# Kernel optimization log

Hardware: AMD Instinct MI355X
Metric: run time of the kernel (lower is better)

The kernel has to match this reference:

```python
import jax, jax.numpy as jnp
from jax import lax
import numpy as np

D = 256      # d_model
E = 512      # d_inner = expand * d_model
N = 16       # m_state
K = 4        # m_conv
R = 16       # dt_rank = ceil(D/16)
H = 8        # n_heads
DK = D // H  # d_keys
B, L = 4, 1024


def setup_inputs() -> dict:
    key = jax.random.key(0)
    ks = jax.random.split(key, 32)
    rn = lambda k, shape, s=0.02: jax.random.normal(k, shape, jnp.float32) * s
    p = {}
    for i, pre in enumerate(['f_', 'b_']):
        o = i * 8
        p[pre + 'Win'] = rn(ks[o], (D, 2 * E))
        p[pre + 'convw'] = rn(ks[o + 1], (E, K), 0.1)
        p[pre + 'convb'] = jnp.zeros((E,), jnp.float32)
        p[pre + 'Wx'] = rn(ks[o + 2], (E, R + 2 * N))
        p[pre + 'Wdt'] = rn(ks[o + 3], (R, E), 0.1)
        p[pre + 'dtb'] = jnp.full((E,), -4.6, jnp.float32)  # softplus(-4.6) ~ 0.01
        p[pre + 'Alog'] = jnp.log(jnp.tile(jnp.arange(1, N + 1, dtype=jnp.float32), (E, 1)))  # (E,N), S4D-real init
        p[pre + 'Dp'] = jnp.ones((E,), jnp.float32)
        p[pre + 'Wout'] = rn(ks[o + 4], (E, D))
    p['Wq'] = rn(ks[20], (D, D))
    p['Wk'] = rn(ks[21], (D, D))
    p['Wv'] = rn(ks[22], (D, D))
    p['Wo'] = rn(ks[23], (D, D))
    p['g_data'] = jax.random.normal(ks[24], (B, L, D), jnp.float32)
    return p


def mamba(x, Win, convw, convb, Wx, Wdt, dtb, Alog, Dp, Wout):
    """Standard Mamba block (in_proj -> causal depthwise conv -> SiLU -> selective scan -> gate -> out_proj)."""
    b = x.shape[0]
    xz = x @ Win                              # (B,L,2E)
    xc, z = xz[..., :E], xz[..., E:]
    # causal depthwise conv over time
    xt = jnp.pad(jnp.swapaxes(xc, 1, 2), ((0, 0), (0, 0), (K - 1, 0)))  # (B,E,L+K-1)
    xt = lax.conv_general_dilated(xt, convw[:, None, :], (1,), 'VALID',
                                  dimension_numbers=('NCH', 'OIH', 'NCH'),
                                  feature_group_count=E)
    xc = jax.nn.silu(jnp.swapaxes(xt + convb[None, :, None], 1, 2))     # (B,L,E)
    # input-dependent SSM params
    xdb = xc @ Wx                             # (B,L,R+2N)
    dt = jax.nn.softplus(xdb[..., :R] @ Wdt + dtb)      # (B,L,E)
    Bm = xdb[..., R:R + N]                    # (B,L,N)
    Cm = xdb[..., R + N:]                     # (B,L,N)
    A = -jnp.exp(Alog)                        # (E,N)
    dA = jnp.exp(dt[..., None] * A)                          # (B,L,E,N)
    dBx = (dt * xc)[..., None] * Bm[:, :, None, :]           # (B,L,E,N)

    def step(h, inp):
        dA_t, dBx_t, C_t = inp
        h = dA_t * h + dBx_t                 # (B,E,N)
        return h, jnp.einsum('ben,bn->be', h, C_t)

    inps = (jnp.swapaxes(dA, 0, 1), jnp.swapaxes(dBx, 0, 1), jnp.swapaxes(Cm, 0, 1))
    h0 = jnp.zeros((b, E, N), x.dtype)
    _, ys = lax.scan(step, h0, inps)          # (L,B,E)
    y = jnp.swapaxes(ys, 0, 1) + xc * Dp
    y = y * jax.nn.silu(z)
    return y @ Wout                           # (B,L,D)


def mha(x, Wq, Wk, Wv, Wo):
    b, l, _ = x.shape
    q = (x @ Wq).reshape(b, l, H, DK)
    k = (x @ Wk).reshape(b, l, H, DK)
    v = (x @ Wv).reshape(b, l, H, DK)
    scores = jnp.einsum('blhd,bshd->bhls', q, k) / jnp.sqrt(jnp.float32(DK))
    attn = jax.nn.softmax(scores, axis=-1)    # mask_flag=False -> no causal mask
    out = jnp.einsum('bhls,bshd->blhd', attn, v).reshape(b, l, D)
    return out @ Wo


def reference(g_data,
              f_Win, f_convw, f_convb, f_Wx, f_Wdt, f_dtb, f_Alog, f_Dp, f_Wout,
              b_Win, b_convw, b_convb, b_Wx, b_Wdt, b_dtb, b_Alog, b_Dp, b_Wout,
              Wq, Wk, Wv, Wo):
    fwd = mamba(g_data, f_Win, f_convw, f_convb, f_Wx, f_Wdt, f_dtb, f_Alog, f_Dp, f_Wout)
    # NOTE: source flips dims=[-1] (feature axis) -- reproduced faithfully
    bwd = jnp.flip(mamba(jnp.flip(g_data, -1), b_Win, b_convw, b_convb, b_Wx, b_Wdt, b_dtb, b_Alog, b_Dp, b_Wout), -1)
    trend = fwd + bwd + g_data
    attn = mha(trend, Wq, Wk, Wv, Wo)
    return jax.nn.gelu(attn)                  # dropout is identity in eval
```

## Files before the change

kernel.cpp:

```cpp
#include <hip/hip_runtime.h>
#include <math.h>

namespace {
typedef unsigned short ushort_t;
constexpr int cL = 1024;

using bf8   = __attribute__((ext_vector_type(8))) short;
using f32x4 = __attribute__((ext_vector_type(4))) float;
using u32x4 = __attribute__((ext_vector_type(4))) unsigned int;
using u32x2 = __attribute__((ext_vector_type(2))) unsigned int;
using fv4   = __attribute__((ext_vector_type(4))) float;

__device__ __forceinline__ float siluf(float x) { return x / (1.f + __expf(-x)); }
__device__ __forceinline__ float softplusf(float x) {
    return fmaxf(x, 0.f) + log1pf(__expf(-fabsf(x)));
}
__device__ __forceinline__ float geluf(float x) {
    float t = tanhf(0.7978845608028654f * (x + 0.044715f * x * x * x));
    return 0.5f * x * (1.f + t);
}
__device__ __forceinline__ ushort_t f2bf(float x) {
    unsigned int u = __float_as_uint(x);
    u = (u + 0x7FFFu + ((u >> 16) & 1u)) >> 16;
    return (ushort_t)u;
}
__device__ __forceinline__ float bf2f(ushort_t h) {
    return __uint_as_float(((unsigned int)h) << 16);
}
__device__ __forceinline__ void nts4(uint4 v, ushort_t* p) {
    u32x4 nv = {v.x, v.y, v.z, v.w};
    __builtin_nontemporal_store(nv, (u32x4*)p);
}
__device__ __forceinline__ void ntsf4(float4 v, float* p) {
    fv4 nv = {v.x, v.y, v.z, v.w};
    __builtin_nontemporal_store(nv, (fv4*)p);
}
__device__ __forceinline__ void nts2(unsigned int a, unsigned int b, ushort_t* p) {
    u32x2 nv = {a, b};
    __builtin_nontemporal_store(nv, (u32x2*)p);
}

enum { EPI_F32 = 0, EPI_GELU = 1, EPI_XZ = 2, EPI_PKS = 3 };

template <int EPI, int BM, int BN, int KS, bool DENSE, bool SW, bool CONVA>
__global__ __launch_bounds__(256)
void mg(const ushort_t* __restrict__ Ah, const ushort_t* __restrict__ Al, size_t sAz,
        const ushort_t* __restrict__ Bh, const ushort_t* __restrict__ Bl, size_t sBz,
        int lda, int ldb, int K,
        float* __restrict__ C, size_t sCz, int ldc, int colmax,
        ushort_t* __restrict__ o0, ushort_t* __restrict__ o1,
        ushort_t* __restrict__ o2, ushort_t* __restrict__ o3, size_t soz,
        const float* __restrict__ cw0, const float* __restrict__ cw1,
        const float* __restrict__ cb0, const float* __restrict__ cb1)
{
    constexpr int MT  = BM / 32;
    constexpr int NTT = BN / 32;
    constexpr int AGR = BM / 64;
    constexpr int BGR = BN / 64;
    __shared__ __align__(16) ushort_t smem[(BM + BN) * 64];
    ushort_t* sAh = smem;
    ushort_t* sAl = smem + BM * 32;
    ushort_t* sBh = smem + BM * 64;
    ushort_t* sBl = smem + BM * 64 + BN * 32;
    const int tid = threadIdx.x;
    const int w = tid >> 6, L = tid & 63, lm = L & 15, lq = L >> 4;
    const int row0 = (SW ? blockIdx.x : blockIdx.y) * BM;
    const int col0 = (SW ? blockIdx.y : blockIdx.x) * BN;
    const int z = blockIdx.z;
    const int dir = (KS == 2) ? (z >> 1) : z;
    const int ks  = (KS == 2) ? (z & 1) : 0;
    const int wm = (w >> 1) * (BM / 2), wn = (w & 1) * (BN / 2);

    size_t aoffs[AGR], boffs[BGR];
    #pragma unroll
    for (int r = 0; r < AGR; ++r) {
        const int G = tid + (r << 8), ar = G >> 2;
        const int sg = (G & 3) ^ ((ar >> 1) & 3);
        aoffs[r] = (size_t)dir * sAz + (size_t)ks * K + (size_t)(row0 + ar) * lda + sg * 8;
    }
    #pragma unroll
    for (int r = 0; r < BGR; ++r) {
        const int G = tid + (r << 8), br = G >> 2;
        const int sg = (G & 3) ^ ((br >> 1) & 3);
        boffs[r] = (size_t)dir * sBz + (size_t)ks * K + (size_t)(col0 + br) * ldb + sg * 8;
    }

    f32x4 acc[MT][NTT];
    #pragma unroll
    for (int i = 0; i < MT; ++i)
        #pragma unroll
        for (int j = 0; j < NTT; ++j) acc[i][j] = (f32x4){0.f, 0.f, 0.f, 0.f};

    if constexpr (CONVA) {
        const float* cw = dir ? cw1 : cw0;
        const float* cb = dir ? cb1 : cb0;
        for (int k0 = 0; k0 < K; k0 += 32) {
            __syncthreads();
            #pragma unroll
            for (int r = 0; r < AGR; ++r) {
                const int G = tid + (r << 8);
                const int ar = G >> 2;
                const int sg = (G & 3) ^ ((ar >> 1) & 3);
                const int e0 = k0 + sg * 8;
                const int grow = row0 + ar;
                const int l = grow & (cL - 1);
                const size_t rb = (size_t)dir * sAz + (size_t)grow * lda + e0;
                uint4 xh4[4], xl4[4];
                #pragma unroll
                for (int j = 0; j < 4; ++j) {
                    if (l + j - 3 >= 0) {
                        xh4[j] = *(const uint4*)(Ah + rb + (ptrdiff_t)(j - 3) * lda);
                        xl4[j] = *(const uint4*)(Al + rb + (ptrdiff_t)(j - 3) * lda);
                    } else {
                        xh4[j] = make_uint4(0, 0, 0, 0);
                        xl4[j] = make_uint4(0, 0, 0, 0);
                    }
                }
                unsigned int hh[4], ll[4];
                #pragma unroll
                for (int i = 0; i < 8; ++i) {
                    float a = cb[e0 + i];
                    const float4 w4 = *(const float4*)&cw[(e0 + i) * 4];
                    const float wj[4] = {w4.x, w4.y, w4.z, w4.w};
                    #pragma unroll
                    for (int j = 0; j < 4; ++j) {
                        const ushort_t hv = ((const ushort_t*)&xh4[j])[i];
                        const ushort_t lv = ((const ushort_t*)&xl4[j])[i];
                        a = fmaf(bf2f(hv) + bf2f(lv), wj[j], a);
                    }
                    const float xc = siluf(a);
                    const ushort_t h = f2bf(xc);
                    const ushort_t lo = f2bf(xc - bf2f(h));
                    if (i & 1) { hh[i >> 1] |= ((unsigned)h) << 16; ll[i >> 1] |= ((unsigned)lo) << 16; }
                    else       { hh[i >> 1] = h;                    ll[i >> 1] = lo; }
                }
                *(uint4*)&sAh[G * 8] = make_uint4(hh[0], hh[1], hh[2], hh[3]);
                *(uint4*)&sAl[G * 8] = make_uint4(ll[0], ll[1], ll[2], ll[3]);
            }
            #pragma unroll
            for (int r = 0; r < BGR; ++r) {
                const int G = tid + (r << 8);
                *(uint4*)&sBh[G * 8] = *(const uint4*)(Bh + boffs[r] + k0);
                *(uint4*)&sBl[G * 8] = *(const uint4*)(Bl + boffs[r] + k0);
            }
            __syncthreads();
            bf8 ah[MT], al[MT], bh[NTT], bl[NTT];
            #pragma unroll
            for (int mt = 0; mt < MT; ++mt) {
                const int rr = wm + mt * 16 + lm;
                const int gx = lq ^ ((rr >> 1) & 3);
                ah[mt] = *(const bf8*)&sAh[rr * 32 + gx * 8];
                al[mt] = *(const bf8*)&sAl[rr * 32 + gx * 8];
            }
            #pragma unroll
            for (int nt = 0; nt < NTT; ++nt) {
                const int rr = wn + nt * 16 + lm;
                const int gx = lq ^ ((rr >> 1) & 3);
                bh[nt] = *(const bf8*)&sBh[rr * 32 + gx * 8];
                bl[nt] = *(const bf8*)&sBl[rr * 32 + gx * 8];
            }
            #pragma unroll
            for (int mt = 0; mt < MT; ++mt)
                #pragma unroll
                for (int nt = 0; nt < NTT; ++nt) {
                    acc[mt][nt] = __builtin_amdgcn_mfma_f32_16x16x32_bf16(ah[mt], bh[nt], acc[mt][nt], 0, 0, 0);
                    acc[mt][nt] = __builtin_amdgcn_mfma_f32_16x16x32_bf16(ah[mt], bl[nt], acc[mt][nt], 0, 0, 0);
                    acc[mt][nt] = __builtin_amdgcn_mfma_f32_16x16x32_bf16(al[mt], bh[nt], acc[mt][nt], 0, 0, 0);
                }
        }
    } else {
        uint4 pa[AGR][2], pb[BGR][2];
        #pragma unroll
        for (int r = 0; r < AGR; ++r) {
            pa[r][0] = *(const uint4*)(Ah + aoffs[r]);
            pa[r][1] = *(const uint4*)(Al + aoffs[r]);
        }
        #pragma unroll
        for (int r = 0; r < BGR; ++r) {
            pb[r][0] = *(const uint4*)(Bh + boffs[r]);
            pb[r][1] = *(const uint4*)(Bl + boffs[r]);
        }
        for (int k0 = 0; k0 < K; k0 += 32) {
            __syncthreads();
            #pragma unroll
            for (int r = 0; r < AGR; ++r) {
                *(uint4*)&sAh[(tid + (r << 8)) * 8] = pa[r][0];
                *(uint4*)&sAl[(tid + (r << 8)) * 8] = pa[r][1];
            }
            #pragma unroll
            for (int r = 0; r < BGR; ++r) {
                *(uint4*)&sBh[(tid + (r << 8)) * 8] = pb[r][0];
                *(uint4*)&sBl[(tid + (r << 8)) * 8] = pb[r][1];
            }
            __syncthreads();
            if (k0 + 32 < K) {
                const int kn = k0 + 32;
                #pragma unroll
                for (int r = 0; r < AGR; ++r) {
                    pa[r][0] = *(const uint4*)(Ah + aoffs[r] + kn);
                    pa[r][1] = *(const uint4*)(Al + aoffs[r] + kn);
                }
                #pragma unroll
                for (int r = 0; r < BGR; ++r) {
                    pb[r][0] = *(const uint4*)(Bh + boffs[r] + kn);
                    pb[r][1] = *(const uint4*)(Bl + boffs[r] + kn);
                }
            }
            bf8 ah[MT], al[MT], bh[NTT], bl[NTT];
            #pragma unroll
            for (int mt = 0; mt < MT; ++mt) {
                const int rr = wm + mt * 16 + lm;
                const int gx = lq ^ ((rr >> 1) & 3);
                ah[mt] = *(const bf8*)&sAh[rr * 32 + gx * 8];
                al[mt] = *(const bf8*)&sAl[rr * 32 + gx * 8];
            }
            #pragma unroll
            for (int nt = 0; nt < NTT; ++nt) {
                const int rr = wn + nt * 16 + lm;
                const int gx = lq ^ ((rr >> 1) & 3);
                bh[nt] = *(const bf8*)&sBh[rr * 32 + gx * 8];
                bl[nt] = *(const bf8*)&sBl[rr * 32 + gx * 8];
            }
            #pragma unroll
            for (int mt = 0; mt < MT; ++mt)
                #pragma unroll
                for (int nt = 0; nt < NTT; ++nt) {
                    acc[mt][nt] = __builtin_amdgcn_mfma_f32_16x16x32_bf16(ah[mt], bh[nt], acc[mt][nt], 0, 0, 0);
                    acc[mt][nt] = __builtin_amdgcn_mfma_f32_16x16x32_bf16(ah[mt], bl[nt], acc[mt][nt], 0, 0, 0);
                    acc[mt][nt] = __builtin_amdgcn_mfma_f32_16x16x32_bf16(al[mt], bh[nt], acc[mt][nt], 0, 0, 0);
                }
        }
    }

    if constexpr (!DENSE) {
        #pragma unroll
        for (int mt = 0; mt < MT; ++mt)
            #pragma unroll
            for (int nt = 0; nt < NTT; ++nt)
                #pragma unroll
                for (int r = 0; r < 4; ++r) {
                    const int row = row0 + wm + mt * 16 + lq * 4 + r;
                    const int col = col0 + wn + nt * 16 + lm;
                    if (col < colmax)
                        C[(size_t)z * sCz + (size_t)row * ldc + col] = acc[mt][nt][r];
                }
    } else {
        constexpr bool isF32 = (EPI == EPI_F32 || EPI == EPI_GELU);
        ushort_t* Eh = smem;
        ushort_t* El = smem + 4096;
        float*    Ef = (float*)smem;
        const bool qsc = (EPI == EPI_PKS) && (col0 < 256);
        #pragma unroll
        for (int mt = 0; mt < MT; ++mt) {
            __syncthreads();
            const int lrb = (w >> 1) * 16 + lq * 4;
            #pragma unroll
            for (int nt = 0; nt < NTT; ++nt) {
                const int cc = wn + nt * 16 + lm;
                #pragma unroll
                for (int r = 0; r < 4; ++r) {
                    float v = acc[mt][nt][r];
                    if (EPI == EPI_GELU) v = geluf(v);
                    if (EPI == EPI_PKS && qsc) v *= 0.17677669529663687f;
                    if (isF32) {
                        Ef[(lrb + r) * 128 + cc] = v;
                    } else {
                        const ushort_t hv = f2bf(v);
                        Eh[(lrb + r) * 128 + cc] = hv;
                        El[(lrb + r) * 128 + cc] = f2bf(v - bf2f(hv));
                    }
                }
            }
            __syncthreads();
            if (isF32) {
                const int j = tid >> 3, part = tid & 7;
                const int grow = row0 + (j >> 4) * (BM / 2) + mt * 16 + (j & 15);
                float* Cz = C + (size_t)z * sCz + (size_t)grow * ldc + col0 + part * 16;
                const float* s = &Ef[j * 128 + part * 16];
                ntsf4(*(const float4*)(s + 0),  Cz + 0);
                ntsf4(*(const float4*)(s + 4),  Cz + 4);
                ntsf4(*(const float4*)(s + 8),  Cz + 8);
                ntsf4(*(const float4*)(s + 12), Cz + 12);
            } else {
                const int p = tid >> 7, u = tid & 127;
                const int j = u >> 2, part = u & 3;
                const int grow = row0 + (j >> 4) * (BM / 2) + mt * 16 + (j & 15);
                const ushort_t* s = (p ? El : Eh) + j * 128 + part * 32;
                ushort_t* D;
                size_t off;
                if (EPI == EPI_XZ) {
                    const bool isx = (col0 < 512);
                    D = isx ? (p ? o1 : o0) : (p ? o3 : o2);
                    off = (size_t)dir * soz + (size_t)grow * 512 + (col0 & 511) + part * 32;
                } else {
                    D = p ? o1 : o0;
                    off = (size_t)grow * ldc + col0 + part * 32;
                }
                nts4(*(const uint4*)(s),      D + off);
                nts4(*(const uint4*)(s + 8),  D + off + 8);
                nts4(*(const uint4*)(s + 16), D + off + 16);
                nts4(*(const uint4*)(s + 24), D + off + 24);
            }
        }
    }
}

__global__ __launch_bounds__(256)
void prep_k(const float* __restrict__ fWin, const float* __restrict__ bWin,
            const float* __restrict__ fWx, const float* __restrict__ bWx,
            const float* __restrict__ fWout, const float* __restrict__ bWout,
            const float* __restrict__ Wq, const float* __restrict__ Wk,
            const float* __restrict__ Wv, const float* __restrict__ Wo,
            const float* __restrict__ g, ushort_t* __restrict__ W,
            ushort_t* __restrict__ gh, ushort_t* __restrict__ gl)
{
    const int i = blockIdx.x * 256 + threadIdx.x;
    float v; ushort_t *dh, *dl;
    if (i < 524288) {
        const int d = i >> 18, j = i & 262143, n = j >> 8, k = j & 255;
        v = d ? bWin[(255 - k) * 1024 + n] : fWin[k * 1024 + n];
        dh = W + d * 524288 + j; dl = dh + 262144;
    } else if (i < 589824) {
        int j = i - 524288; const int d = j >> 15; j &= 32767;
        const int n = j >> 9, k = j & 511;
        const float* Wx = d ? bWx : fWx;
        v = (n < 48) ? Wx[k * 48 + n] : 0.f;
        dh = W + 1048576 + d * 65536 + j; dl = dh + 32768;
    } else if (i < 851968) {
        int j = i - 589824; const int d = j >> 17; j &= 131071;
        const int n = j >> 9, k = j & 511;
        v = d ? bWout[k * 256 + (255 - n)] : fWout[k * 256 + n];
        dh = W + 1179648 + d * 262144 + j; dl = dh + 131072;
    } else if (i < 1048576) {
        const int j = i - 851968, n = j >> 8, k = j & 255;
        v = (n < 256) ? Wq[k * 256 + n] : (n < 512) ? Wk[k * 256 + n - 256] : Wv[k * 256 + n - 512];
        dh = W + 1703936 + j; dl = dh + 196608;
    } else if (i < 1114112) {
        const int j = i - 1048576, n = j >> 8, k = j & 255;
        v = Wo[k * 256 + n];
        dh = W + 2097152 + j; dl = dh + 65536;
    } else {
        const int j = i - 1114112;
        v = g[j];
        dh = gh + j; dl = gl + j;
    }
    const ushort_t hv = f2bf(v);
    *dh = hv; *dl = f2bf(v - bf2f(hv));
}

__global__ __launch_bounds__(256)
void scan_p1(const float* __restrict__ xdb, const ushort_t* __restrict__ xpk,
             const float* __restrict__ fWdt, const float* __restrict__ bWdt,
             const float* __restrict__ fdtb, const float* __restrict__ bdtb,
             const float* __restrict__ fcw, const float* __restrict__ bcw,
             const float* __restrict__ fcb, const float* __restrict__ bcb,
             float* __restrict__ P, float* __restrict__ He)
{
    const int bid = blockIdx.x;
    const int ehalf = bid & 1, c = (bid >> 1) & 31, b = (bid >> 6) & 3, dir = bid >> 8;
    const int e = (ehalf << 8) + threadIdx.x;
    const float* Wdt = dir ? bWdt : fWdt;
    const float dtbias = (dir ? bdtb : fdtb)[e];
    const float4 cw4 = *(const float4*)((dir ? bcw : fcw) + e * 4);
    const float cbias = (dir ? bcb : fcb)[e];
    float wdt[16];
    #pragma unroll
    for (int r = 0; r < 16; ++r) wdt[r] = Wdt[r * 512 + e];
    const ushort_t* xh = xpk + (size_t)dir * 4194304 + e;
    const ushort_t* xl = xh + 2097152;
    const float* xrow = xdb + (size_t)dir * 196608;
    const int t0 = c * 32, rowb = b * cL;
    float x0 = 0.f, x1 = 0.f, x2 = 0.f;
    if (t0 >= 3) {
        x0 = bf2f(xh[(size_t)(rowb + t0 - 3) * 512]) + bf2f(xl[(size_t)(rowb + t0 - 3) * 512]);
        x1 = bf2f(xh[(size_t)(rowb + t0 - 2) * 512]) + bf2f(xl[(size_t)(rowb + t0 - 2) * 512]);
        x2 = bf2f(xh[(size_t)(rowb + t0 - 1) * 512]) + bf2f(xl[(size_t)(rowb + t0 - 1) * 512]);
    }
    float h[16], p[16];
    #pragma unroll
    for (int n = 0; n < 16; ++n) { h[n] = 0.f; p[n] = 1.f; }
    #pragma unroll 2
    for (int t = t0; t < t0 + 32; ++t) {
        const int row = rowb + t;
        const float* rp = xrow + (size_t)row * 48;
        float dtr = dtbias;
        #pragma unroll
        for (int j = 0; j < 16; ++j) dtr = fmaf(rp[j], wdt[j], dtr);
        const float dtv = softplusf(dtr);
        const float x3 = bf2f(xh[(size_t)row * 512]) + bf2f(xl[(size_t)row * 512]);
        const float xv = siluf(cbias + cw4.x * x0 + cw4.y * x1 + cw4.z * x2 + cw4.w * x3);
        x0 = x1; x1 = x2; x2 = x3;
        const float dx = dtv * xv;
        const float r = __expf(-dtv);
        float da = 1.f;
        #pragma unroll
        for (int n = 0; n < 16; ++n) {
            da *= r;
            h[n] = fmaf(da, h[n], dx * rp[16 + n]);
            p[n] *= da;
        }
    }
    const size_t base = ((((size_t)dir * 4 + b) * 512 + e) * 32 + c) * 16;
    #pragma unroll
    for (int n = 0; n < 16; ++n) { P[base + n] = p[n]; He[base + n] = h[n]; }
}

__global__ __launch_bounds__(256)
void scan_p2(float* __restrict__ P, const float* __restrict__ He)
{
    const int g = blockIdx.x * 256 + threadIdx.x;
    const int n = g & 15, be = g >> 4;
    const size_t base = (size_t)be * 512 + n;
    float run = 0.f;
    for (int c = 0; c < 32; ++c) {
        const size_t o = base + (size_t)c * 16;
        const float pv = P[o], he = He[o];
        P[o] = run;
        run = fmaf(pv, run, he);
    }
}

__global__ __launch_bounds__(256)
void scan_p3(const float* __restrict__ xdb, const ushort_t* __restrict__ xpk,
             const float* __restrict__ fWdt, const float* __restrict__ bWdt,
             const float* __restrict__ fdtb, const float* __restrict__ bdtb,
             const float* __restrict__ fcw, const float* __restrict__ bcw,
             const float* __restrict__ fcb, const float* __restrict__ bcb,
             const float* __restrict__ fDp, const float* __restrict__ bDp,
             const float* __restrict__ H0, ushort_t* __restrict__ zpk)
{
    const int bid = blockIdx.x;
    const int ehalf = bid & 1, c = (bid >> 1) & 31, b = (bid >> 6) & 3, dir = bid >> 8;
    const int e = (ehalf << 8) + threadIdx.x;
    const float* Wdt = dir ? bWdt : fWdt;
    const float dtbias = (dir ? bdtb : fdtb)[e];
    const float dpe = (dir ? bDp : fDp)[e];
    const float4 cw4 = *(const float4*)((dir ? bcw : fcw) + e * 4);
    const float cbias = (dir ? bcb : fcb)[e];
    float wdt[16];
    #pragma unroll
    for (int r = 0; r < 16; ++r) wdt[r] = Wdt[r * 512 + e];
    const ushort_t* xh = xpk + (size_t)dir * 4194304 + e;
    const ushort_t* xl = xh + 2097152;
    ushort_t* zh = zpk + (size_t)dir * 4194304 + e;
    ushort_t* zl = zh + 2097152;
    const float* xrow = xdb + (size_t)dir * 196608;
    const int t0 = c * 32, rowb = b * cL;
    float x0 = 0.f, x1 = 0.f, x2 = 0.f;
    if (t0 >= 3) {
        x0 = bf2f(xh[(size_t)(rowb + t0 - 3) * 512]) + bf2f(xl[(size_t)(rowb + t0 - 3) * 512]);
        x1 = bf2f(xh[(size_t)(rowb + t0 - 2) * 512]) + bf2f(xl[(size_t)(rowb + t0 - 2) * 512]);
        x2 = bf2f(xh[(size_t)(rowb + t0 - 1) * 512]) + bf2f(xl[(size_t)(rowb + t0 - 1) * 512]);
    }
    float h[16];
    const size_t base = ((((size_t)dir * 4 + b) * 512 + e) * 32 + c) * 16;
    #pragma unroll
    for (int n = 0; n < 16; ++n) h[n] = H0[base + n];
    #pragma unroll 2
    for (int t = t0; t < t0 + 32; ++t) {
        const int row = rowb + t;
        const float* rp = xrow + (size_t)row * 48;
        float dtr = dtbias;
        #pragma unroll
        for (int j = 0; j < 16; ++j) dtr = fmaf(rp[j], wdt[j], dtr);
        const float dtv = softplusf(dtr);
        const float x3 = bf2f(xh[(size_t)row * 512]) + bf2f(xl[(size_t)row * 512]);
        const float xv = siluf(cbias + cw4.x * x0 + cw4.y * x1 + cw4.z * x2 + cw4.w * x3);
        x0 = x1; x1 = x2; x2 = x3;
        const float dx = dtv * xv;
        const float r = __expf(-dtv);
        float da = 1.f, acc = 0.f;
        #pragma unroll
        for (int n = 0; n < 16; ++n) {
            da *= r;
            h[n] = fmaf(da, h[n], dx * rp[16 + n]);
            acc = fmaf(h[n], rp[32 + n], acc);
        }
        const size_t zo = (size_t)row * 512;
        const float zv = bf2f(zh[zo]) + bf2f(zl[zo]);
        const float y = (acc + xv * dpe) * siluf(zv);
        const ushort_t hv = f2bf(y);
        zh[zo] = hv; zl[zo] = f2bf(y - bf2f(hv));
    }
}

__global__ __launch_bounds__(256)
void addtrend_k(const float* __restrict__ outp, const float* __restrict__ g,
                ushort_t* __restrict__ th, ushort_t* __restrict__ tl)
{
    const int i4 = blockIdx.x * 256 + threadIdx.x;
    float4 s = ((const float4*)g)[i4];
    #pragma unroll
    for (int ss = 0; ss < 4; ++ss) {
        const float4 t = ((const float4*)(outp + (size_t)ss * 1048576))[i4];
        s.x += t.x; s.y += t.y; s.z += t.z; s.w += t.w;
    }
    const float v[4] = {s.x, s.y, s.z, s.w};
    unsigned int hw[2], lw[2];
    #pragma unroll
    for (int j = 0; j < 2; ++j) {
        const ushort_t h0 = f2bf(v[2*j]),     h1 = f2bf(v[2*j+1]);
        const ushort_t l0 = f2bf(v[2*j]   - bf2f(h0));
        const ushort_t l1 = f2bf(v[2*j+1] - bf2f(h1));
        hw[j] = (unsigned)h0 | ((unsigned)h1 << 16);
        lw[j] = (unsigned)l0 | ((unsigned)l1 << 16);
    }
    nts2(hw[0], hw[1], &th[(size_t)i4 * 4]);
    nts2(lw[0], lw[1], &tl[(size_t)i4 * 4]);
}

__global__ __launch_bounds__(256)
void attn_mf(const ushort_t* __restrict__ qh, const ushort_t* __restrict__ ql,
             ushort_t* __restrict__ aoh, ushort_t* __restrict__ aol)
{
    constexpr int QS = 40, PS = 72, VS = 72;
    __shared__ ushort_t Qh[128 * QS], Ql[128 * QS];
    __shared__ ushort_t Kh[64 * QS],  Kl[64 * QS];
    __shared__ ushort_t Vh[32 * VS],  Vl[32 * VS];
    __shared__ __align__(16) ushort_t Ps[128 * PS];
    const int tid = threadIdx.x;
    const int qt = blockIdx.x, bh = blockIdx.y;
    const int b = bh >> 3, h = bh & 7;
    const int w = tid >> 6, L = tid & 63, lm = L & 15, lq = L >> 4;
    const size_t rowb = (size_t)b * cL;

    {
        const int r = tid >> 1, c0 = (tid & 1) << 4;
        const size_t src = (rowb + qt * 128 + r) * 768 + h * 32 + c0;
        *(uint4*)&Qh[r * QS + c0]     = *(const uint4*)(qh + src);
        *(uint4*)&Qh[r * QS + c0 + 8] = *(const uint4*)(qh + src + 8);
        *(uint4*)&Ql[r * QS + c0]     = *(const uint4*)(ql + src);
        *(uint4*)&Ql[r * QS + c0 + 8] = *(const uint4*)(ql + src + 8);
    }
    __syncthreads();
    bf8 qhf[2], qlf[2];
    #pragma unroll
    for (int mt = 0; mt < 2; ++mt) {
        qhf[mt] = *(const bf8*)&Qh[(w * 32 + mt * 16 + lm) * QS + lq * 8];
        qlf[mt] = *(const bf8*)&Ql[(w * 32 + mt * 16 + lm) * QS + lq * 8];
    }

    f32x4 oc[2][2];
    float rs[2][4];
    #pragma unroll
    for (int mt = 0; mt < 2; ++mt) {
        #pragma unroll
        for (int d = 0; d < 2; ++d) oc[mt][d] = (f32x4){0.f, 0.f, 0.f, 0.f};
        #pragma unroll
        for (int r = 0; r < 4; ++r) rs[mt][r] = 0.f;
    }

    for (int kt = 0; kt < 16; ++kt) {
        __syncthreads();
        {
            const int r = tid >> 2, c0 = (tid & 3) << 3;
            const size_t src = (rowb + kt * 64 + r) * 768 + 256 + h * 32 + c0;
            *(uint4*)&Kh[r * QS + c0] = *(const uint4*)(qh + src);
            *(uint4*)&Kl[r * QS + c0] = *(const uint4*)(ql + src);
        }
        {
            const int key = tid >> 2, c0 = (tid & 3) << 3;
            const size_t src = (rowb + kt * 64 + key) * 768 + 512 + h * 32 + c0;
            const uint4 vh4 = *(const uint4*)(qh + src);
            const uint4 vl4 = *(const uint4*)(ql + src);
            const ushort_t* vhp = (const ushort_t*)&vh4;
            const ushort_t* vlp = (const ushort_t*)&vl4;
            #pragma unroll
            for (int j = 0; j < 8; ++j) {
                Vh[(c0 + j) * VS + key] = vhp[j];
                Vl[(c0 + j) * VS + key] = vlp[j];
            }
        }
        __syncthreads();
        bf8 khf[4], klf[4];
        #pragma unroll
        for (int nt = 0; nt < 4; ++nt) {
            khf[nt] = *(const bf8*)&Kh[(nt * 16 + lm) * QS + lq * 8];
            klf[nt] = *(const bf8*)&Kl[(nt * 16 + lm) * QS + lq * 8];
        }
        f32x4 sc[2][4];
        #pragma unroll
        for (int mt = 0; mt < 2; ++mt)
            #pragma unroll
            for (int nt = 0; nt < 4; ++nt) {
                f32x4 a = (f32x4){0.f, 0.f, 0.f, 0.f};
                a = __builtin_amdgcn_mfma_f32_16x16x32_bf16(qhf[mt], khf[nt], a, 0, 0, 0);
                a = __builtin_amdgcn_mfma_f32_16x16x32_bf16(qhf[mt], klf[nt], a, 0, 0, 0);
                a = __builtin_amdgcn_mfma_f32_16x16x32_bf16(qlf[mt], khf[nt], a, 0, 0, 0);
                sc[mt][nt] = a;
            }
        #pragma unroll
        for (int mt = 0; mt < 2; ++mt) {
            float part[4] = {0.f, 0.f, 0.f, 0.f};
            #pragma unroll
            for (int nt = 0; nt < 4; ++nt)
                #pragma unroll
                for (int r = 0; r < 4; ++r) {
                    const float p = __expf(sc[mt][nt][r]);
                    part[r] += p;
                    Ps[(w * 32 + mt * 16 + lq * 4 + r) * PS + nt * 16 + lm] = f2bf(p);
                }
            #pragma unroll
            for (int r = 0; r < 4; ++r) {
                float v = part[r];
                #pragma unroll
                for (int d = 1; d < 16; d <<= 1) v += __shfl_xor(v, d, 64);
                rs[mt][r] += v;
            }
        }
        bf8 pf[2][2], vhf[2][2], vlf[2][2];
        #pragma unroll
        for (int mt = 0; mt < 2; ++mt)
            #pragma unroll
            for (int ks = 0; ks < 2; ++ks)
                pf[mt][ks] = *(const bf8*)&Ps[(w * 32 + mt * 16 + lm) * PS + ks * 32 + lq * 8];
        #pragma unroll
        for (int dkt = 0; dkt < 2; ++dkt)
            #pragma unroll
            for (int ks = 0; ks < 2; ++ks) {
                vhf[dkt][ks] = *(const bf8*)&Vh[(dkt * 16 + lm) * VS + ks * 32 + lq * 8];
                vlf[dkt][ks] = *(const bf8*)&Vl[(dkt * 16 + lm) * VS + ks * 32 + lq * 8];
            }
        #pragma unroll
        for (int mt = 0; mt < 2; ++mt)
            #pragma unroll
            for (int dkt = 0; dkt < 2; ++dkt)
                #pragma unroll
                for (int ks = 0; ks < 2; ++ks) {
                    oc[mt][dkt] = __builtin_amdgcn_mfma_f32_16x16x32_bf16(pf[mt][ks], vhf[dkt][ks], oc[mt][dkt], 0, 0, 0);
                    oc[mt][dkt] = __builtin_amdgcn_mfma_f32_16x16x32_bf16(pf[mt][ks], vlf[dkt][ks], oc[mt][dkt], 0, 0, 0);
                }
    }
    __syncthreads();
    #pragma unroll
    for (int mt = 0; mt < 2; ++mt)
        #pragma unroll
        for (int r = 0; r < 4; ++r) {
            const float inv = 1.f / rs[mt][r];
            const int lrow = w * 32 + mt * 16 + lq * 4 + r;
            #pragma unroll
            for (int dkt = 0; dkt < 2; ++dkt) {
                const float v = oc[mt][dkt][r] * inv;
                const ushort_t hv = f2bf(v);
                Ps[lrow * 64 + dkt * 16 + lm] = hv;
                Ps[lrow * 64 + 32 + dkt * 16 + lm] = f2bf(v - bf2f(hv));
            }
        }
    __syncthreads();
    {
        const int row = tid >> 1, half = tid & 1;
        const ushort_t* s = &Ps[row * 64 + half * 32];
        ushort_t* dst = (half ? aol : aoh) + (rowb + qt * 128 + row) * 256 + h * 32;
        nts4(*(const uint4*)(s),      dst);
        nts4(*(const uint4*)(s + 8),  dst + 8);
        nts4(*(const uint4*)(s + 16), dst + 16);
        nts4(*(const uint4*)(s + 24), dst + 24);
    }
}
}

extern "C" void kernel_launch(void* const* d_in, const int* in_sizes, int n_in,
                              void* d_out, int out_size, void* d_ws, size_t ws_size,
                              hipStream_t stream)
{
    (void)in_sizes; (void)n_in; (void)out_size; (void)ws_size;
    const float* fWin  = (const float*)d_in[0];
    const float* fconvw= (const float*)d_in[1];
    const float* fconvb= (const float*)d_in[2];
    const float* fWx   = (const float*)d_in[3];
    const float* fWdt  = (const float*)d_in[4];
    const float* fdtb  = (const float*)d_in[5];
    const float* fDp   = (const float*)d_in[7];
    const float* fWout = (const float*)d_in[8];
    const float* bWin  = (const float*)d_in[9];
    const float* bconvw= (const float*)d_in[10];
    const float* bconvb= (const float*)d_in[11];
    const float* bWx   = (const float*)d_in[12];
    const float* bWdt  = (const float*)d_in[13];
    const float* bdtb  = (const float*)d_in[14];
    const float* bDp   = (const float*)d_in[16];
    const float* bWout = (const float*)d_in[17];
    const float* Wq = (const float*)d_in[18];
    const float* Wk = (const float*)d_in[19];
    const float* Wv = (const float*)d_in[20];
    const float* Wo = (const float*)d_in[21];
    const float* g  = (const float*)d_in[22];

    float* wsF = (float*)d_ws;
    ushort_t* wpk = (ushort_t*)wsF;
    ushort_t* xh  = (ushort_t*)(wsF + 1114112);
    ushort_t* zh  = (ushort_t*)(wsF + 5308416);
    float*    P   = wsF + 9502720;
    float*    He  = wsF + 11599872;
    ushort_t* gh  = (ushort_t*)(wsF + 9502720);
    ushort_t* gl  = gh + 1048576;
    float*    outp = wsF + 9502720;
    ushort_t* th  = (ushort_t*)(wsF + 1114112);
    ushort_t* tl  = th + 1048576;
    ushort_t* qkvh = th + 2097152;
    ushort_t* qkvl = th + 5242880;
    ushort_t* aoh = (ushort_t*)(wsF + 5308416);
    ushort_t* aol = aoh + 1048576;
    float*    xdbF = wsF + 13697024;

    const dim3 blk(256);
    prep_k<<<dim3(8448), blk, 0, stream>>>(fWin, bWin, fWx, bWx, fWout, bWout,
                                           Wq, Wk, Wv, Wo, g, wpk, gh, gl);
    mg<EPI_XZ, 128, 128, 1, true, true, false><<<dim3(32, 8, 2), blk, 0, stream>>>(
        gh, gl, 0, wpk, wpk + 262144, 524288, 256, 256, 256,
        nullptr, 0, 0, 0, xh, xh + 2097152, zh, zh + 2097152, 4194304,
        nullptr, nullptr, nullptr, nullptr);
    mg<EPI_F32, 128, 64, 1, false, false, true><<<dim3(1, 32, 2), blk, 0, stream>>>(
        xh, xh + 2097152, 4194304, wpk + 1048576, wpk + 1081344, 65536, 512, 512, 512,
        xdbF, 196608, 48, 48, nullptr, nullptr, nullptr, nullptr, 0,
        fconvw, bconvw, fconvb, bconvb);
    scan_p1<<<dim3(512), blk, 0, stream>>>(xdbF, xh, fWdt, bWdt, fdtb, bdtb,
                                           fconvw, bconvw, fconvb, bconvb, P, He);
    scan_p2<<<dim3(256), blk, 0, stream>>>(P, He);
    scan_p3<<<dim3(512), blk, 0, stream>>>(xdbF, xh, fWdt, bWdt, fdtb, bdtb,
                                           fconvw, bconvw, fconvb, bconvb, fDp, bDp, P, zh);
    mg<EPI_F32, 128, 128, 2, true, false, false><<<dim3(2, 32, 4), blk, 0, stream>>>(
        zh, zh + 2097152, 4194304, wpk + 1179648, wpk + 1310720, 262144, 512, 512, 256,
        outp, 1048576, 256, 256, nullptr, nullptr, nullptr, nullptr, 0,
        nullptr, nullptr, nullptr, nullptr);
    addtrend_k<<<dim3(1024), blk, 0, stream>>>(outp, g, th, tl);
    mg<EPI_PKS, 64, 128, 1, true, false, false><<<dim3(6, 64, 1), blk, 0, stream>>>(
        th, tl, 0, wpk + 1703936, wpk + 1900544, 0, 256, 256, 256,
        nullptr, 0, 768, 768, qkvh, qkvl, nullptr, nullptr, 0,
        nullptr, nullptr, nullptr, nullptr);
    attn_mf<<<dim3(8, 32), blk, 0, stream>>>(qkvh, qkvl, aoh, aol);
    mg<EPI_GELU, 64, 128, 1, true, false, false><<<dim3(2, 64, 1), blk, 0, stream>>>(
        aoh, aol, 0, wpk + 2097152, wpk + 2162688, 0, 256, 256, 256,
        (float*)d_out, 0, 256, 256, nullptr, nullptr, nullptr, nullptr, 0,
        nullptr, nullptr, nullptr, nullptr);
}
```

Baseline: 498.3 us.

## Split-K the conv+x_proj GEMM, shrink tiles, pad epilogue LDS, drop nontemporal stores

The conv-fused x_proj GEMM is now split four ways along K, giving 8 z-slices and 64-row tiles, and writes partial sums into a scratch buffer. A new reduction kernel adds the partials into xdbF. The in_proj and out_proj GEMMs drop to 64-row tiles, doubling their block counts. Epilogue LDS strides are padded (136/132) to avoid bank conflicts, and nontemporal stores become ordinary stores. The intent is more parallelism on a small, under-occupied GEMM, paid for with an extra launch and partial-sum traffic; the partial buffer reuses workspace that overlaps gh/gl, which looks unused by then.

```diff
diff --git a/kernel.cpp b/kernel.cpp
--- a/kernel.cpp
+++ b/kernel.cpp
@@ -7,9 +7,6 @@
 
 using bf8   = __attribute__((ext_vector_type(8))) short;
 using f32x4 = __attribute__((ext_vector_type(4))) float;
-using u32x4 = __attribute__((ext_vector_type(4))) unsigned int;
-using u32x2 = __attribute__((ext_vector_type(2))) unsigned int;
-using fv4   = __attribute__((ext_vector_type(4))) float;
 
 __device__ __forceinline__ float siluf(float x) { return x / (1.f + __expf(-x)); }
 __device__ __forceinline__ float softplusf(float x) {
@@ -26,18 +23,6 @@
 }
 __device__ __forceinline__ float bf2f(ushort_t h) {
     return __uint_as_float(((unsigned int)h) << 16);
-}
-__device__ __forceinline__ void nts4(uint4 v, ushort_t* p) {
-    u32x4 nv = {v.x, v.y, v.z, v.w};
-    __builtin_nontemporal_store(nv, (u32x4*)p);
-}
-__device__ __forceinline__ void ntsf4(float4 v, float* p) {
-    fv4 nv = {v.x, v.y, v.z, v.w};
-    __builtin_nontemporal_store(nv, (fv4*)p);
-}
-__device__ __forceinline__ void nts2(unsigned int a, unsigned int b, ushort_t* p) {
-    u32x2 nv = {a, b};
-    __builtin_nontemporal_store(nv, (u32x2*)p);
 }
 
 enum { EPI_F32 = 0, EPI_GELU = 1, EPI_XZ = 2, EPI_PKS = 3 };
@@ -57,6 +42,8 @@
     constexpr int NTT = BN / 32;
     constexpr int AGR = BM / 64;
     constexpr int BGR = BN / 64;
+    constexpr int ESH = 136;
+    constexpr int ESF = 132;
     __shared__ __align__(16) ushort_t smem[(BM + BN) * 64];
     ushort_t* sAh = smem;
     ushort_t* sAl = smem + BM * 32;
@@ -67,17 +54,11 @@
     const int row0 = (SW ? blockIdx.x : blockIdx.y) * BM;
     const int col0 = (SW ? blockIdx.y : blockIdx.x) * BN;
     const int z = blockIdx.z;
-    const int dir = (KS == 2) ? (z >> 1) : z;
-    const int ks  = (KS == 2) ? (z & 1) : 0;
+    const int dir = (KS == 1) ? z : ((KS == 2) ? (z >> 1) : (z >> 2));
+    const int ks  = (KS == 1) ? 0 : ((KS == 2) ? (z & 1) : (z & 3));
     const int wm = (w >> 1) * (BM / 2), wn = (w & 1) * (BN / 2);
 
-    size_t aoffs[AGR], boffs[BGR];
-    #pragma unroll
-    for (int r = 0; r < AGR; ++r) {
-        const int G = tid + (r << 8), ar = G >> 2;
-        const int sg = (G & 3) ^ ((ar >> 1) & 3);
-        aoffs[r] = (size_t)dir * sAz + (size_t)ks * K + (size_t)(row0 + ar) * lda + sg * 8;
-    }
+    size_t boffs[BGR];
     #pragma unroll
     for (int r = 0; r < BGR; ++r) {
         const int G = tid + (r << 8), br = G >> 2;
@@ -101,10 +82,10 @@
                 const int G = tid + (r << 8);
                 const int ar = G >> 2;
                 const int sg = (G & 3) ^ ((ar >> 1) & 3);
-                const int e0 = k0 + sg * 8;
+                const int eg = ks * K + k0 + sg * 8;
                 const int grow = row0 + ar;
                 const int l = grow & (cL - 1);
-                const size_t rb = (size_t)dir * sAz + (size_t)grow * lda + e0;
+                const size_t rb = (size_t)dir * sAz + (size_t)grow * lda + eg;
                 uint4 xh4[4], xl4[4];
                 #pragma unroll
                 for (int j = 0; j < 4; ++j) {
@@ -119,8 +100,8 @@
                 unsigned int hh[4], ll[4];
                 #pragma unroll
                 for (int i = 0; i < 8; ++i) {
-                    float a = cb[e0 + i];
-                    const float4 w4 = *(const float4*)&cw[(e0 + i) * 4];
+                    float a = cb[eg + i];
+                    const float4 w4 = *(const float4*)&cw[(eg + i) * 4];
                     const float wj[4] = {w4.x, w4.y, w4.z, w4.w};
                     #pragma unroll
                     for (int j = 0; j < 4; ++j) {
@@ -169,6 +150,13 @@
                 }
         }
     } else {
+        size_t aoffs[AGR];
+        #pragma unroll
+        for (int r = 0; r < AGR; ++r) {
+            const int G = tid + (r << 8), ar = G >> 2;
+            const int sg = (G & 3) ^ ((ar >> 1) & 3);
+            aoffs[r] = (size_t)dir * sAz + (size_t)ks * K + (size_t)(row0 + ar) * lda + sg * 8;
+        }
         uint4 pa[AGR][2], pb[BGR][2];
         #pragma unroll
         for (int r = 0; r < AGR; ++r) {
@@ -247,7 +235,7 @@
     } else {
         constexpr bool isF32 = (EPI == EPI_F32 || EPI == EPI_GELU);
         ushort_t* Eh = smem;
-        ushort_t* El = smem + 4096;
+        ushort_t* El = smem + 32 * ESH;
         float*    Ef = (float*)smem;
         const bool qsc = (EPI == EPI_PKS) && (col0 < 256);
         #pragma unroll
@@ -263,11 +251,11 @@
                     if (EPI == EPI_GELU) v = geluf(v);
                     if (EPI == EPI_PKS && qsc) v *= 0.17677669529663687f;
                     if (isF32) {
-                        Ef[(lrb + r) * 128 + cc] = v;
+                        Ef[(lrb + r) * ESF + cc] = v;
                     } else {
                         const ushort_t hv = f2bf(v);
-                        Eh[(lrb + r) * 128 + cc] = hv;
-                        El[(lrb + r) * 128 + cc] = f2bf(v - bf2f(hv));
+                        Eh[(lrb + r) * ESH + cc] = hv;
+                        El[(lrb + r) * ESH + cc] = f2bf(v - bf2f(hv));
                     }
                 }
             }
@@ -276,16 +264,16 @@
                 const int j = tid >> 3, part = tid & 7;
                 const int grow = row0 + (j >> 4) * (BM / 2) + mt * 16 + (j & 15);
                 float* Cz = C + (size_t)z * sCz + (size_t)grow * ldc + col0 + part * 16;
-                const float* s = &Ef[j * 128 + part * 16];
-                ntsf4(*(const float4*)(s + 0),  Cz + 0);
-                ntsf4(*(const float4*)(s + 4),  Cz + 4);
-                ntsf4(*(const float4*)(s + 8),  Cz + 8);
-                ntsf4(*(const float4*)(s + 12), Cz + 12);
+                const float* s = &Ef[j * ESF + part * 16];
+                *(float4*)(Cz + 0)  = *(const float4*)(s + 0);
+                *(float4*)(Cz + 4)  = *(const float4*)(s + 4);
+                *(float4*)(Cz + 8)  = *(const float4*)(s + 8);
+                *(float4*)(Cz + 12) = *(const float4*)(s + 12);
             } else {
                 const int p = tid >> 7, u = tid & 127;
                 const int j = u >> 2, part = u & 3;
                 const int grow = row0 + (j >> 4) * (BM / 2) + mt * 16 + (j & 15);
-                const ushort_t* s = (p ? El : Eh) + j * 128 + part * 32;
+                const ushort_t* s = (p ? El : Eh) + j * ESH + part * 32;
                 ushort_t* D;
                 size_t off;
                 if (EPI == EPI_XZ) {
@@ -296,13 +284,27 @@
                     D = p ? o1 : o0;
                     off = (size_t)grow * ldc + col0 + part * 32;
                 }
-                nts4(*(const uint4*)(s),      D + off);
-                nts4(*(const uint4*)(s + 8),  D + off + 8);
-                nts4(*(const uint4*)(s + 16), D + off + 16);
-                nts4(*(const uint4*)(s + 24), D + off + 24);
-            }
-        }
-    }
+                *(uint4*)(D + off)      = *(const uint4*)(s);
+                *(uint4*)(D + off + 8)  = *(const uint4*)(s + 8);
+                *(uint4*)(D + off + 16) = *(const uint4*)(s + 16);
+                *(uint4*)(D + off + 24) = *(const uint4*)(s + 24);
+            }
+        }
+    }
+}
+
+__global__ __launch_bounds__(256)
+void xdbred_k(const float* __restrict__ parts, float* __restrict__ out)
+{
+    const int i = blockIdx.x * 256 + threadIdx.x;
+    const int c = i % 48;
+    const int row = (i / 48) & 4095;
+    const int dir = i / (48 * 4096);
+    float s = 0.f;
+    #pragma unroll
+    for (int ks = 0; ks < 4; ++ks)
+        s += parts[(size_t)(dir * 4 + ks) * 262144 + (size_t)row * 64 + c];
+    out[(size_t)dir * 196608 + (size_t)row * 48 + c] = s;
 }
 
 __global__ __launch_bounds__(256)
@@ -505,8 +507,8 @@
         hw[j] = (unsigned)h0 | ((unsigned)h1 << 16);
         lw[j] = (unsigned)l0 | ((unsigned)l1 << 16);
     }
-    nts2(hw[0], hw[1], &th[(size_t)i4 * 4]);
-    nts2(lw[0], lw[1], &tl[(size_t)i4 * 4]);
+    *(uint2*)&th[(size_t)i4 * 4] = make_uint2(hw[0], hw[1]);
+    *(uint2*)&tl[(size_t)i4 * 4] = make_uint2(lw[0], lw[1]);
 }
 
 __global__ __launch_bounds__(256)
@@ -651,10 +653,10 @@
         const int row = tid >> 1, half = tid & 1;
         const ushort_t* s = &Ps[row * 64 + half * 32];
         ushort_t* dst = (half ? aol : aoh) + (rowb + qt * 128 + row) * 256 + h * 32;
-        nts4(*(const uint4*)(s),      dst);
-        nts4(*(const uint4*)(s + 8),  dst + 8);
-        nts4(*(const uint4*)(s + 16), dst + 16);
-        nts4(*(const uint4*)(s + 24), dst + 24);
+        *(uint4*)(dst)      = *(const uint4*)(s);
+        *(uint4*)(dst + 8)  = *(const uint4*)(s + 8);
+        *(uint4*)(dst + 16) = *(const uint4*)(s + 16);
+        *(uint4*)(dst + 24) = *(const uint4*)(s + 24);
     }
 }
 }
@@ -694,6 +696,7 @@
     float*    He  = wsF + 11599872;
     ushort_t* gh  = (ushort_t*)(wsF + 9502720);
     ushort_t* gl  = gh + 1048576;
+    float*    xdbp = wsF + 9502720;
     float*    outp = wsF + 9502720;
     ushort_t* th  = (ushort_t*)(wsF + 1114112);
     ushort_t* tl  = th + 1048576;
@@ -706,20 +709,21 @@
     const dim3 blk(256);
     prep_k<<<dim3(8448), blk, 0, stream>>>(fWin, bWin, fWx, bWx, fWout, bWout,
                                            Wq, Wk, Wv, Wo, g, wpk, gh, gl);
-    mg<EPI_XZ, 128, 128, 1, true, true, false><<<dim3(32, 8, 2), blk, 0, stream>>>(
+    mg<EPI_XZ, 64, 128, 1, true, true, false><<<dim3(64, 8, 2), blk, 0, stream>>>(
         gh, gl, 0, wpk, wpk + 262144, 524288, 256, 256, 256,
         nullptr, 0, 0, 0, xh, xh + 2097152, zh, zh + 2097152, 4194304,
         nullptr, nullptr, nullptr, nullptr);
-    mg<EPI_F32, 128, 64, 1, false, false, true><<<dim3(1, 32, 2), blk, 0, stream>>>(
-        xh, xh + 2097152, 4194304, wpk + 1048576, wpk + 1081344, 65536, 512, 512, 512,
-        xdbF, 196608, 48, 48, nullptr, nullptr, nullptr, nullptr, 0,
+    mg<EPI_F32, 64, 64, 4, false, false, true><<<dim3(1, 64, 8), blk, 0, stream>>>(
+        xh, xh + 2097152, 4194304, wpk + 1048576, wpk + 1081344, 65536, 512, 512, 128,
+        xdbp, 262144, 64, 64, nullptr, nullptr, nullptr, nullptr, 0,
         fconvw, bconvw, fconvb, bconvb);
+    xdbred_k<<<dim3(1536), blk, 0, stream>>>(xdbp, xdbF);
     scan_p1<<<dim3(512), blk, 0, stream>>>(xdbF, xh, fWdt, bWdt, fdtb, bdtb,
                                            fconvw, bconvw, fconvb, bconvb, P, He);
     scan_p2<<<dim3(256), blk, 0, stream>>>(P, He);
     scan_p3<<<dim3(512), blk, 0, stream>>>(xdbF, xh, fWdt, bWdt, fdtb, bdtb,
                                            fconvw, bconvw, fconvb, bconvb, fDp, bDp, P, zh);
-    mg<EPI_F32, 128, 128, 2, true, false, false><<<dim3(2, 32, 4), blk, 0, stream>>>(
+    mg<EPI_F32, 64, 128, 2, true, false, false><<<dim3(2, 64, 4), blk, 0, stream>>>(
         zh, zh + 2097152, 4194304, wpk + 1179648, wpk + 1310720, 262144, 512, 512, 256,
         outp, 1048576, 256, 256, nullptr, nullptr, nullptr, nullptr, 0,
         nullptr, nullptr, nullptr, nullptr);
```

Result: faster. 414.6 us (-16.8%).
